# Optimization experiments

Hardware: AMD Instinct MI355X
Metric: run time of the kernel (lower is better)

Reference implementation:

```python
import jax, jax.numpy as jnp
import numpy as np

H, KVH, DH = 16, 4, 128
EPS = 1e-8

def _rmsnorm(t, gamma):
    # normalize over last dim (dim_head)
    ms = jnp.mean(t * t, axis=-1, keepdims=True)
    return t * jax.lax.rsqrt(ms + EPS) * gamma

def setup_inputs() -> dict:
    key = jax.random.key(0)
    ks = jax.random.split(key, 5)
    d = H * DH  # 2048
    kv_d = KVH * DH  # 512
    x = jax.random.normal(ks[0], (2, 2048, d), dtype=jnp.float32)
    Wq = jax.random.normal(ks[1], (d, d), dtype=jnp.float32) * (d ** -0.5)
    Wk = jax.random.normal(ks[2], (d, kv_d), dtype=jnp.float32) * (d ** -0.5)
    Wv = jax.random.normal(ks[3], (d, kv_d), dtype=jnp.float32) * (d ** -0.5)
    Wo = jax.random.normal(ks[4], (d, d), dtype=jnp.float32) * (d ** -0.5)
    q_gamma = jnp.ones((DH,), dtype=jnp.float32)
    k_gamma = jnp.ones((DH,), dtype=jnp.float32)
    return {"x": x, "Wq": Wq, "Wk": Wk, "Wv": Wv, "Wo": Wo,
            "q_gamma": q_gamma, "k_gamma": k_gamma}

def reference(x, Wq, Wk, Wv, Wo, q_gamma, k_gamma):
    b, s, d = x.shape
    g = H // KVH  # GQA group size
    q = (x @ Wq).reshape(b, s, H, DH)
    k = (x @ Wk).reshape(b, s, KVH, DH)
    v = (x @ Wv).reshape(b, s, KVH, DH)
    # fused QK RMSNorm (per-head, over dim_head)
    q = _rmsnorm(q, q_gamma)
    k = _rmsnorm(k, k_gamma)
    # GQA: expand kv heads across query-head groups
    k = jnp.repeat(k, g, axis=2)  # [b, s, H, DH]
    v = jnp.repeat(v, g, axis=2)
    scores = jnp.einsum('bqhd,bkhd->bhqk', q, k) * (DH ** -0.5)
    causal = jnp.tril(jnp.ones((s, s), dtype=bool))
    scores = jnp.where(causal, scores, jnp.finfo(scores.dtype).min)
    attn = jax.nn.softmax(scores, axis=-1)
    out = jnp.einsum('bhqk,bkhd->bqhd', attn, v).reshape(b, s, H * DH)
    out = out @ Wo
    return out + x  # residual skip
```

## Files before the change

### kernel.cpp

```cpp
#include <hip/hip_runtime.h>

typedef unsigned short u16;
typedef __attribute__((ext_vector_type(8))) short short8;
typedef __attribute__((ext_vector_type(4))) float f32x4;

#define DEVI __device__ __forceinline__

DEVI float u2f(u16 u) {
    unsigned int x = ((unsigned int)u) << 16;
    float f; __builtin_memcpy(&f, &x, 4); return f;
}
DEVI u16 f2u(float f) {
    unsigned int x; __builtin_memcpy(&x, &f, 4);
    x = (x + 0x7fffu + ((x >> 16) & 1u)) >> 16;
    return (u16)x;
}
DEVI void gld16(const u16* g, u16* ldsbase) {
    __builtin_amdgcn_global_load_lds(
        (const __attribute__((address_space(1))) unsigned int*)g,
        (__attribute__((address_space(3))) unsigned int*)ldsbase, 16, 0, 0);
}

__global__ __launch_bounds__(256) void cvt_bf16(
    const float* __restrict__ x, u16* __restrict__ xb, int n)
{
    int g = (blockIdx.x * 256 + threadIdx.x) * 8;
    float4 a = *(const float4*)&x[g];
    float4 b = *(const float4*)&x[g + 4];
    short8 v;
    v[0]=(short)f2u(a.x); v[1]=(short)f2u(a.y); v[2]=(short)f2u(a.z); v[3]=(short)f2u(a.w);
    v[4]=(short)f2u(b.x); v[5]=(short)f2u(b.y); v[6]=(short)f2u(b.z); v[7]=(short)f2u(b.w);
    *(short8*)&xb[g] = v;
}

__global__ __launch_bounds__(256) void transpose_all(
    const float* __restrict__ Wq, const float* __restrict__ Wk,
    const float* __restrict__ Wv, const float* __restrict__ Wo,
    u16* __restrict__ WTqkv, u16* __restrict__ WoT)
{
    __shared__ u16 T[64 * 72];
    int id = blockIdx.x;
    const float* W; u16* WT; int N, bx, by;
    if (id < 1024)      {            W = Wo; WT = WoT;   N = 2048; bx = id & 31; by = id >> 5; }
    else if (id < 2048) { id -= 1024; W = Wq; WT = WTqkv; N = 2048; bx = id & 31; by = id >> 5; }
    else if (id < 2304) { id -= 2048; W = Wk; WT = WTqkv + (size_t)2048 * 2048; N = 512; bx = id & 7; by = id >> 3; }
    else                { id -= 2304; W = Wv; WT = WTqkv + (size_t)2560 * 2048; N = 512; bx = id & 7; by = id >> 3; }
    const int K = 2048;
    const int tid = threadIdx.x;
    const int k0 = by * 64, n0 = bx * 64;
#pragma unroll
    for (int i = 0; i < 2; ++i) {
        int c = tid + i * 256;
        int row = c >> 3, n8 = (c & 7) * 8;
        const float* src = &W[(size_t)(k0 + row) * N + n0 + n8];
#pragma unroll
        for (int j = 0; j < 8; ++j)
            T[(n8 + j) * 72 + row] = f2u(src[j]);
    }
    __syncthreads();
#pragma unroll
    for (int i = 0; i < 2; ++i) {
        int c = tid + i * 256;
        int n = c >> 3, k8 = (c & 7) * 8;
        *(short8*)&WT[(size_t)(n0 + n) * K + k0 + k8] = *(const short8*)&T[n * 72 + k8];
    }
}

__global__ __launch_bounds__(256) void gemm_lds(
    const u16* __restrict__ A, int lda,
    const u16* __restrict__ WT,
    void* __restrict__ C, int ldc, const float* __restrict__ resid, int c_f32,
    int M, int N, int K,
    const float* __restrict__ qg, const float* __restrict__ kg, int fuse_norm)
{
    __shared__ u16 As[128 * 32];
    __shared__ u16 Bs[128 * 32];
    const int tid = threadIdx.x;
    const int lane = tid & 63, w = tid >> 6;
    const int wm = w >> 1, wn = w & 1;
    const int l15 = lane & 15, quad = lane >> 4;
    const int r4 = lane >> 2, c4 = (lane & 3) * 8;
    const int m0 = blockIdx.y * 128, n0 = blockIdx.x * 128;

    f32x4 acc[4][4] = {};
    for (int k0 = 0; k0 < K; k0 += 32) {
#pragma unroll
        for (int j = 0; j < 2; ++j) {
            int row = w * 32 + j * 16;
            gld16(&WT[(size_t)(n0 + row + r4) * K + k0 + c4], &Bs[row * 32]);
            gld16(&A [(size_t)(m0 + row + r4) * lda + k0 + c4], &As[row * 32]);
        }
        __syncthreads();
        short8 a[4], b[4];
#pragma unroll
        for (int mt = 0; mt < 4; ++mt)
            a[mt] = *(const short8*)&As[(wm * 64 + mt * 16 + l15) * 32 + quad * 8];
#pragma unroll
        for (int nt = 0; nt < 4; ++nt)
            b[nt] = *(const short8*)&Bs[(wn * 64 + nt * 16 + l15) * 32 + quad * 8];
#pragma unroll
        for (int mt = 0; mt < 4; ++mt)
#pragma unroll
            for (int nt = 0; nt < 4; ++nt)
                acc[mt][nt] = __builtin_amdgcn_mfma_f32_16x16x32_bf16(a[mt], b[nt], acc[mt][nt], 0, 0, 0);
        __syncthreads();
    }

    if (fuse_norm && n0 < 2560) {
        const float* gamma = (n0 < 2048) ? qg : kg;
        float* red = (float*)As;
#pragma unroll
        for (int mt = 0; mt < 4; ++mt)
#pragma unroll
            for (int r = 0; r < 4; ++r) {
                float p = 0.f;
#pragma unroll
                for (int nt = 0; nt < 4; ++nt) p += acc[mt][nt][r] * acc[mt][nt][r];
#pragma unroll
                for (int msk = 1; msk < 16; msk <<= 1) p += __shfl_xor(p, msk);
                if (l15 == 0)
                    red[(wm * 64 + mt * 16 + quad * 4 + r) * 2 + wn] = p;
            }
        __syncthreads();
        float gv[4];
#pragma unroll
        for (int nt = 0; nt < 4; ++nt) gv[nt] = gamma[wn * 64 + nt * 16 + l15];
#pragma unroll
        for (int mt = 0; mt < 4; ++mt)
#pragma unroll
            for (int r = 0; r < 4; ++r) {
                int rl = wm * 64 + mt * 16 + quad * 4 + r;
                float m2 = red[rl * 2] + red[rl * 2 + 1];
                float sc = rsqrtf(m2 * (1.0f / 128.0f) + 1e-8f);
#pragma unroll
                for (int nt = 0; nt < 4; ++nt) acc[mt][nt][r] *= sc * gv[nt];
            }
    }

#pragma unroll
    for (int mt = 0; mt < 4; ++mt) {
#pragma unroll
        for (int r = 0; r < 4; ++r) {
            int row = m0 + wm * 64 + mt * 16 + quad * 4 + r;
#pragma unroll
            for (int nt = 0; nt < 4; ++nt) {
                int col = n0 + wn * 64 + nt * 16 + l15;
                float v = acc[mt][nt][r];
                if (resid) v += resid[(size_t)row * ldc + col];
                if (c_f32) ((float*)C)[(size_t)row * ldc + col] = v;
                else       ((u16*)C)[(size_t)row * ldc + col] = f2u(v);
            }
        }
    }
}

__global__ __launch_bounds__(256) void vtrans(
    const u16* __restrict__ qkv, u16* __restrict__ vT)
{
    __shared__ u16 T[128 * 72];
    const int tid = threadIdx.x;
    const int t0 = blockIdx.x * 64;
    const int kvh = blockIdx.y, b = blockIdx.z;
#pragma unroll
    for (int i = 0; i < 4; ++i) {
        int c = tid + i * 256;
        int tl = c >> 4, d8 = (c & 15) * 8;
        short8 v = *(const short8*)&qkv[(size_t)(b * 2048 + t0 + tl) * 3072 + 2560 + kvh * 128 + d8];
#pragma unroll
        for (int j = 0; j < 8; ++j)
            T[(d8 + j) * 72 + tl] = (u16)v[j];
    }
    __syncthreads();
#pragma unroll
    for (int i = 0; i < 4; ++i) {
        int c = tid + i * 256;
        int d = c >> 3, t8 = (c & 7) * 8;
        *(short8*)&vT[((size_t)(b * 4 + kvh) * 128 + d) * 2048 + t0 + t8] =
            *(const short8*)&T[d * 72 + t8];
    }
}

#define QS 136
#define VS 72
__global__ __launch_bounds__(256) void attn(
    u16* __restrict__ qkv, const u16* __restrict__ vT)
{
    __shared__ u16 lds[27136];
    u16* const Ks  = lds;
    u16* const Vs  = lds + 8704;
    u16* const Psb[2] = { lds + 17920, lds + 22528 };
    u16* const Qsb[2] = { lds + 8704, lds + 17408 };

    const int tid = threadIdx.x, lane = tid & 63, w = tid >> 6;
    const int l15 = lane & 15, quad = lane >> 4;
    const int h = blockIdx.y, b = blockIdx.z;
    const int kvh = h >> 2;
    const int qts[2] = { (int)blockIdx.x, 31 - (int)blockIdx.x };
    const float scale = 0.08838834764831845f;

#pragma unroll
    for (int t = 0; t < 2; ++t)
#pragma unroll
        for (int i = 0; i < 4; ++i) {
            int c = tid + i * 256;
            int r = c >> 4, d8 = (c & 15) * 8;
            *(short8*)&Qsb[t][r * QS + d8] =
                *(const short8*)&qkv[(size_t)(b * 2048 + qts[t] * 64 + r) * 3072 + h * 128 + d8];
        }
    __syncthreads();
    short8 qf[2][4];
#pragma unroll
    for (int t = 0; t < 2; ++t)
#pragma unroll
        for (int ks = 0; ks < 4; ++ks)
            qf[t][ks] = *(const short8*)&Qsb[t][(w * 16 + l15) * QS + ks * 32 + quad * 8];
    __syncthreads();

    f32x4 o[2][8] = {};
    float mrow[2][4], lrow[2][4];
#pragma unroll
    for (int t = 0; t < 2; ++t)
#pragma unroll
        for (int r = 0; r < 4; ++r) { mrow[t][r] = -1e30f; lrow[t][r] = 0.f; }

    for (int kt = 0; kt <= qts[1]; ++kt) {
        const int kv0 = kt * 64;
#pragma unroll
        for (int i = 0; i < 4; ++i) {
            int c = tid + i * 256;
            int r = c >> 4, d8 = (c & 15) * 8;
            *(short8*)&Ks[r * QS + d8] =
                *(const short8*)&qkv[(size_t)(b * 2048 + kv0 + r) * 3072 + 2048 + kvh * 128 + d8];
        }
#pragma unroll
        for (int i = 0; i < 4; ++i) {
            int c = tid + i * 256;
            int d = c >> 3, t8 = (c & 7) * 8;
            *(short8*)&Vs[d * VS + t8] =
                *(const short8*)&vT[((size_t)(b * 4 + kvh) * 128 + d) * 2048 + kv0 + t8];
        }
        __syncthreads();

#pragma unroll
        for (int t = 0; t < 2; ++t) {
            if (kt > qts[t]) continue;
            f32x4 s[4];
#pragma unroll
            for (int nt = 0; nt < 4; ++nt) {
                f32x4 a = {};
#pragma unroll
                for (int ks = 0; ks < 4; ++ks) {
                    short8 bk = *(const short8*)&Ks[(nt * 16 + l15) * QS + ks * 32 + quad * 8];
                    a = __builtin_amdgcn_mfma_f32_16x16x32_bf16(qf[t][ks], bk, a, 0, 0, 0);
                }
                s[nt] = a;
            }
            const bool diag = (kt == qts[t]);
#pragma unroll
            for (int nt = 0; nt < 4; ++nt) {
                int col = nt * 16 + l15;
#pragma unroll
                for (int r = 0; r < 4; ++r) {
                    float v = s[nt][r] * scale;
                    if (diag) {
                        int row = w * 16 + quad * 4 + r;
                        if (col > row) v = -1e30f;
                    }
                    s[nt][r] = v;
                }
            }
            float alpha[4];
#pragma unroll
            for (int r = 0; r < 4; ++r) {
                float mx = s[0][r];
#pragma unroll
                for (int nt = 1; nt < 4; ++nt) mx = fmaxf(mx, s[nt][r]);
#pragma unroll
                for (int msk = 1; msk < 16; msk <<= 1) mx = fmaxf(mx, __shfl_xor(mx, msk));
                float mn = fmaxf(mrow[t][r], mx);
                alpha[r] = __expf(mrow[t][r] - mn);
                mrow[t][r] = mn;
            }
#pragma unroll
            for (int r = 0; r < 4; ++r) {
                float sum = 0.f;
#pragma unroll
                for (int nt = 0; nt < 4; ++nt) {
                    float p = __expf(s[nt][r] - mrow[t][r]);
                    s[nt][r] = p;
                    sum += p;
                }
#pragma unroll
                for (int msk = 1; msk < 16; msk <<= 1) sum += __shfl_xor(sum, msk);
                lrow[t][r] = lrow[t][r] * alpha[r] + sum;
            }
#pragma unroll
            for (int nt = 0; nt < 4; ++nt)
#pragma unroll
                for (int r = 0; r < 4; ++r)
                    Psb[t][(w * 16 + quad * 4 + r) * VS + nt * 16 + l15] = f2u(s[nt][r]);
#pragma unroll
            for (int nto = 0; nto < 8; ++nto)
#pragma unroll
                for (int r = 0; r < 4; ++r)
                    o[t][nto][r] *= alpha[r];
        }
        __syncthreads();

#pragma unroll
        for (int t = 0; t < 2; ++t) {
            if (kt > qts[t]) continue;
            short8 pa[2];
#pragma unroll
            for (int ks = 0; ks < 2; ++ks)
                pa[ks] = *(const short8*)&Psb[t][(w * 16 + l15) * VS + ks * 32 + quad * 8];
#pragma unroll
            for (int nto = 0; nto < 8; ++nto) {
#pragma unroll
                for (int ks = 0; ks < 2; ++ks) {
                    short8 bv = *(const short8*)&Vs[(nto * 16 + l15) * VS + ks * 32 + quad * 8];
                    o[t][nto] = __builtin_amdgcn_mfma_f32_16x16x32_bf16(pa[ks], bv, o[t][nto], 0, 0, 0);
                }
            }
        }
        __syncthreads();
    }
#pragma unroll
    for (int t = 0; t < 2; ++t)
#pragma unroll
        for (int r = 0; r < 4; ++r) {
            float inv = 1.0f / lrow[t][r];
            int row = qts[t] * 64 + w * 16 + quad * 4 + r;
#pragma unroll
            for (int nto = 0; nto < 8; ++nto)
                qkv[(size_t)(b * 2048 + row) * 3072 + h * 128 + nto * 16 + l15] =
                    f2u(o[t][nto][r] * inv);
        }
}

extern "C" void kernel_launch(void* const* d_in, const int* in_sizes, int n_in,
                              void* d_out, int out_size, void* d_ws, size_t ws_size,
                              hipStream_t stream) {
    const float* x  = (const float*)d_in[0];
    const float* Wq = (const float*)d_in[1];
    const float* Wk = (const float*)d_in[2];
    const float* Wv = (const float*)d_in[3];
    const float* Wo = (const float*)d_in[4];
    const float* qg = (const float*)d_in[5];
    const float* kg = (const float*)d_in[6];

    char* ws = (char*)d_ws;
    u16* WoT   = (u16*)(ws);
    u16* QKV   = (u16*)(ws + 8388608);
    u16* vT    = (u16*)(ws + 33554432);
    u16* WTqkv = (u16*)(ws + 33554432);
    u16* xbf   = (u16*)d_out;

    cvt_bf16<<<dim3(4096), 256, 0, stream>>>(x, xbf, 8388608);

    transpose_all<<<dim3(2560), 256, 0, stream>>>(Wq, Wk, Wv, Wo, WTqkv, WoT);

    gemm_lds<<<dim3(24, 32), 256, 0, stream>>>(xbf, 2048, WTqkv, QKV, 3072,
                                               nullptr, 0, 4096, 3072, 2048,
                                               qg, kg, 1);

    vtrans<<<dim3(32, 4, 2), 256, 0, stream>>>(QKV, vT);

    attn<<<dim3(16, 16, 2), 256, 0, stream>>>(QKV, vT);

    gemm_lds<<<dim3(16, 32), 256, 0, stream>>>(QKV, 3072, WoT, d_out, 2048,
                                               x, 1, 4096, 2048, 2048,
                                               nullptr, nullptr, 0);
}
```

Measured before the change: 371.8 us.

## Compute transposed S in attention and pass P through registers, merge prep kernels

The attention kernel now computes S^T (K as the A operand, Q as B), so each lane holds one query row's scores. The row max and row sum need only two cross-lane shuffles, and the P tile is packed to bf16 and rearranged with shuffles into the A-operand layout for the PV MFMA. This removes the LDS round trip for P and one __syncthreads per KV tile, and lowers LDS use, which may raise occupancy. Separately, the bf16 conversion of x and the weight transposes are merged into a single prep launch to save one kernel launch. The risks are extra shuffle and permute instruction overhead and subtle layout mistakes in the operand remap.

```diff
diff --git a/kernel.cpp b/kernel.cpp
--- a/kernel.cpp
+++ b/kernel.cpp
@@ -15,38 +15,41 @@
     x = (x + 0x7fffu + ((x >> 16) & 1u)) >> 16;
     return (u16)x;
 }
+DEVI unsigned int fbits(float f) {
+    unsigned int x; __builtin_memcpy(&x, &f, 4); return x;
+}
 DEVI void gld16(const u16* g, u16* ldsbase) {
     __builtin_amdgcn_global_load_lds(
         (const __attribute__((address_space(1))) unsigned int*)g,
         (__attribute__((address_space(3))) unsigned int*)ldsbase, 16, 0, 0);
 }
 
-__global__ __launch_bounds__(256) void cvt_bf16(
-    const float* __restrict__ x, u16* __restrict__ xb, int n)
-{
-    int g = (blockIdx.x * 256 + threadIdx.x) * 8;
-    float4 a = *(const float4*)&x[g];
-    float4 b = *(const float4*)&x[g + 4];
-    short8 v;
-    v[0]=(short)f2u(a.x); v[1]=(short)f2u(a.y); v[2]=(short)f2u(a.z); v[3]=(short)f2u(a.w);
-    v[4]=(short)f2u(b.x); v[5]=(short)f2u(b.y); v[6]=(short)f2u(b.z); v[7]=(short)f2u(b.w);
-    *(short8*)&xb[g] = v;
-}
-
-__global__ __launch_bounds__(256) void transpose_all(
+__global__ __launch_bounds__(256) void prep(
+    const float* __restrict__ x,
     const float* __restrict__ Wq, const float* __restrict__ Wk,
     const float* __restrict__ Wv, const float* __restrict__ Wo,
-    u16* __restrict__ WTqkv, u16* __restrict__ WoT)
+    u16* __restrict__ xbf, u16* __restrict__ WTqkv, u16* __restrict__ WoT)
 {
     __shared__ u16 T[64 * 72];
     int id = blockIdx.x;
+    const int tid = threadIdx.x;
+    if (id < 4096) {
+        int g = (id * 256 + tid) * 8;
+        float4 a = *(const float4*)&x[g];
+        float4 c = *(const float4*)&x[g + 4];
+        short8 v;
+        v[0]=(short)f2u(a.x); v[1]=(short)f2u(a.y); v[2]=(short)f2u(a.z); v[3]=(short)f2u(a.w);
+        v[4]=(short)f2u(c.x); v[5]=(short)f2u(c.y); v[6]=(short)f2u(c.z); v[7]=(short)f2u(c.w);
+        *(short8*)&xbf[g] = v;
+        return;
+    }
+    id -= 4096;
     const float* W; u16* WT; int N, bx, by;
     if (id < 1024)      {            W = Wo; WT = WoT;   N = 2048; bx = id & 31; by = id >> 5; }
     else if (id < 2048) { id -= 1024; W = Wq; WT = WTqkv; N = 2048; bx = id & 31; by = id >> 5; }
     else if (id < 2304) { id -= 2048; W = Wk; WT = WTqkv + (size_t)2048 * 2048; N = 512; bx = id & 7; by = id >> 3; }
     else                { id -= 2304; W = Wv; WT = WTqkv + (size_t)2560 * 2048; N = 512; bx = id & 7; by = id >> 3; }
     const int K = 2048;
-    const int tid = threadIdx.x;
     const int k0 = by * 64, n0 = bx * 64;
 #pragma unroll
     for (int i = 0; i < 2; ++i) {
@@ -185,11 +188,9 @@
 __global__ __launch_bounds__(256) void attn(
     u16* __restrict__ qkv, const u16* __restrict__ vT)
 {
-    __shared__ u16 lds[27136];
-    u16* const Ks  = lds;
-    u16* const Vs  = lds + 8704;
-    u16* const Psb[2] = { lds + 17920, lds + 22528 };
-    u16* const Qsb[2] = { lds + 8704, lds + 17408 };
+    __shared__ u16 lds[17920];
+    u16* const Ks = lds;
+    u16* const Vs = lds + 8704;
 
     const int tid = threadIdx.x, lane = tid & 63, w = tid >> 6;
     const int l15 = lane & 15, quad = lane >> 4;
@@ -204,7 +205,7 @@
         for (int i = 0; i < 4; ++i) {
             int c = tid + i * 256;
             int r = c >> 4, d8 = (c & 15) * 8;
-            *(short8*)&Qsb[t][r * QS + d8] =
+            *(short8*)&lds[t * 8704 + r * QS + d8] =
                 *(const short8*)&qkv[(size_t)(b * 2048 + qts[t] * 64 + r) * 3072 + h * 128 + d8];
         }
     __syncthreads();
@@ -213,15 +214,11 @@
     for (int t = 0; t < 2; ++t)
 #pragma unroll
         for (int ks = 0; ks < 4; ++ks)
-            qf[t][ks] = *(const short8*)&Qsb[t][(w * 16 + l15) * QS + ks * 32 + quad * 8];
+            qf[t][ks] = *(const short8*)&lds[t * 8704 + (w * 16 + l15) * QS + ks * 32 + quad * 8];
     __syncthreads();
 
     f32x4 o[2][8] = {};
-    float mrow[2][4], lrow[2][4];
-#pragma unroll
-    for (int t = 0; t < 2; ++t)
-#pragma unroll
-        for (int r = 0; r < 4; ++r) { mrow[t][r] = -1e30f; lrow[t][r] = 0.f; }
+    float m_[2] = { -1e30f, -1e30f }, l_[2] = { 0.f, 0.f };
 
     for (int kt = 0; kt <= qts[1]; ++kt) {
         const int kv0 = kt * 64;
@@ -250,92 +247,98 @@
                 f32x4 a = {};
 #pragma unroll
                 for (int ks = 0; ks < 4; ++ks) {
-                    short8 bk = *(const short8*)&Ks[(nt * 16 + l15) * QS + ks * 32 + quad * 8];
-                    a = __builtin_amdgcn_mfma_f32_16x16x32_bf16(qf[t][ks], bk, a, 0, 0, 0);
+                    short8 kf = *(const short8*)&Ks[(nt * 16 + l15) * QS + ks * 32 + quad * 8];
+                    a = __builtin_amdgcn_mfma_f32_16x16x32_bf16(kf, qf[t][ks], a, 0, 0, 0);
                 }
                 s[nt] = a;
             }
-            const bool diag = (kt == qts[t]);
-#pragma unroll
-            for (int nt = 0; nt < 4; ++nt) {
-                int col = nt * 16 + l15;
+            if (kt == qts[t]) {
+                int qrow = w * 16 + l15;
+#pragma unroll
+                for (int nt = 0; nt < 4; ++nt)
+#pragma unroll
+                    for (int r = 0; r < 4; ++r) {
+                        float v = s[nt][r] * scale;
+                        if (nt * 16 + quad * 4 + r > qrow) v = -1e30f;
+                        s[nt][r] = v;
+                    }
+            } else {
+#pragma unroll
+                for (int nt = 0; nt < 4; ++nt)
+#pragma unroll
+                    for (int r = 0; r < 4; ++r) s[nt][r] *= scale;
+            }
+            float mx = s[0][0];
+#pragma unroll
+            for (int nt = 0; nt < 4; ++nt)
+#pragma unroll
+                for (int r = 0; r < 4; ++r) mx = fmaxf(mx, s[nt][r]);
+            mx = fmaxf(mx, __shfl_xor(mx, 16));
+            mx = fmaxf(mx, __shfl_xor(mx, 32));
+            float mn = fmaxf(m_[t], mx);
+            float alpha = __expf(m_[t] - mn);
+            m_[t] = mn;
+            float sum = 0.f;
+#pragma unroll
+            for (int nt = 0; nt < 4; ++nt)
 #pragma unroll
                 for (int r = 0; r < 4; ++r) {
-                    float v = s[nt][r] * scale;
-                    if (diag) {
-                        int row = w * 16 + quad * 4 + r;
-                        if (col > row) v = -1e30f;
-                    }
-                    s[nt][r] = v;
-                }
-            }
-            float alpha[4];
-#pragma unroll
-            for (int r = 0; r < 4; ++r) {
-                float mx = s[0][r];
-#pragma unroll
-                for (int nt = 1; nt < 4; ++nt) mx = fmaxf(mx, s[nt][r]);
-#pragma unroll
-                for (int msk = 1; msk < 16; msk <<= 1) mx = fmaxf(mx, __shfl_xor(mx, msk));
-                float mn = fmaxf(mrow[t][r], mx);
-                alpha[r] = __expf(mrow[t][r] - mn);
-                mrow[t][r] = mn;
-            }
-#pragma unroll
-            for (int r = 0; r < 4; ++r) {
-                float sum = 0.f;
-#pragma unroll
-                for (int nt = 0; nt < 4; ++nt) {
-                    float p = __expf(s[nt][r] - mrow[t][r]);
+                    float p = __expf(s[nt][r] - mn);
                     s[nt][r] = p;
                     sum += p;
                 }
-#pragma unroll
-                for (int msk = 1; msk < 16; msk <<= 1) sum += __shfl_xor(sum, msk);
-                lrow[t][r] = lrow[t][r] * alpha[r] + sum;
-            }
+            sum += __shfl_xor(sum, 16);
+            sum += __shfl_xor(sum, 32);
+            l_[t] = l_[t] * alpha + sum;
+            unsigned int pk[4][2];
 #pragma unroll
             for (int nt = 0; nt < 4; ++nt)
 #pragma unroll
-                for (int r = 0; r < 4; ++r)
-                    Psb[t][(w * 16 + quad * 4 + r) * VS + nt * 16 + l15] = f2u(s[nt][r]);
-#pragma unroll
-            for (int nto = 0; nto < 8; ++nto)
-#pragma unroll
-                for (int r = 0; r < 4; ++r)
-                    o[t][nto][r] *= alpha[r];
-        }
-        __syncthreads();
-
-#pragma unroll
-        for (int t = 0; t < 2; ++t) {
-            if (kt > qts[t]) continue;
-            short8 pa[2];
-#pragma unroll
-            for (int ks = 0; ks < 2; ++ks)
-                pa[ks] = *(const short8*)&Psb[t][(w * 16 + l15) * VS + ks * 32 + quad * 8];
+                for (int i = 0; i < 2; ++i)
+                    pk[nt][i] = __builtin_amdgcn_perm(
+                        fbits(s[nt][2 * i + 1]), fbits(s[nt][2 * i]), 0x07060302u);
+            int af[2][4];
+#pragma unroll
+            for (int c = 0; c < 2; ++c)
+#pragma unroll
+                for (int d = 0; d < 4; ++d) {
+                    int src = l15 + 16 * ((quad & 1) * 2 + (d >> 1));
+                    int v0 = __shfl((int)pk[2 * c][d & 1], src);
+                    int v1 = __shfl((int)pk[2 * c + 1][d & 1], src);
+                    af[c][d] = (quad >= 2) ? v1 : v0;
+                }
+            union { int i4[4]; short8 s8; } ua0, ua1;
+#pragma unroll
+            for (int d = 0; d < 4; ++d) { ua0.i4[d] = af[0][d]; ua1.i4[d] = af[1][d]; }
+#pragma unroll
+            for (int r = 0; r < 4; ++r) {
+                float ao = __shfl(alpha, quad * 4 + r);
+#pragma unroll
+                for (int nto = 0; nto < 8; ++nto) o[t][nto][r] *= ao;
+            }
 #pragma unroll
             for (int nto = 0; nto < 8; ++nto) {
-#pragma unroll
-                for (int ks = 0; ks < 2; ++ks) {
-                    short8 bv = *(const short8*)&Vs[(nto * 16 + l15) * VS + ks * 32 + quad * 8];
-                    o[t][nto] = __builtin_amdgcn_mfma_f32_16x16x32_bf16(pa[ks], bv, o[t][nto], 0, 0, 0);
-                }
-            }
-        }
-        __syncthreads();
-    }
-#pragma unroll
-    for (int t = 0; t < 2; ++t)
+                short8 bv0 = *(const short8*)&Vs[(nto * 16 + l15) * VS + quad * 8];
+                short8 bv1 = *(const short8*)&Vs[(nto * 16 + l15) * VS + 32 + quad * 8];
+                o[t][nto] = __builtin_amdgcn_mfma_f32_16x16x32_bf16(ua0.s8, bv0, o[t][nto], 0, 0, 0);
+                o[t][nto] = __builtin_amdgcn_mfma_f32_16x16x32_bf16(ua1.s8, bv1, o[t][nto], 0, 0, 0);
+            }
+        }
+        __syncthreads();
+    }
+#pragma unroll
+    for (int t = 0; t < 2; ++t) {
+        float rl = 1.0f / l_[t];
 #pragma unroll
         for (int r = 0; r < 4; ++r) {
-            float inv = 1.0f / lrow[t][r];
+            float inv = __shfl(rl, quad * 4 + r);
             int row = qts[t] * 64 + w * 16 + quad * 4 + r;
 #pragma unroll
             for (int nto = 0; nto < 8; ++nto)
                 qkv[(size_t)(b * 2048 + row) * 3072 + h * 128 + nto * 16 + l15] =
                     f2u(o[t][nto][r] * inv);
         }
+    }
 }
 
 extern "C" void kernel_launch(void* const* d_in, const int* in_sizes, int n_in,
@@ -356,9 +359,7 @@
     u16* WTqkv = (u16*)(ws + 33554432);
     u16* xbf   = (u16*)d_out;
 
-    cvt_bf16<<<dim3(4096), 256, 0, stream>>>(x, xbf, 8388608);
-
-    transpose_all<<<dim3(2560), 256, 0, stream>>>(Wq, Wk, Wv, Wo, WTqkv, WoT);
+    prep<<<dim3(6656), 256, 0, stream>>>(x, Wq, Wk, Wv, Wo, xbf, WTqkv, WoT);
 
     gemm_lds<<<dim3(24, 32), 256, 0, stream>>>(xbf, 2048, WTqkv, QKV, 3072,
                                                nullptr, 0, 4096, 3072, 2048,
```

Measured after the change: 354.4 us. 4.7% less time.
